# Kernel tuning notes

Measured on AMD Instinct MI355X. Metric: run time of the kernel, lower is better.

Reference implementation:

```python
import jax, jax.numpy as jnp
import numpy as np

EPS = 1e-8  # torch F.cosine_similarity eps


def _cosine_logits(emb, mem):
    # emb: [N, C], mem: [S, C] -> [N, S]
    num = emb @ mem.T
    denom = jnp.linalg.norm(emb, axis=1, keepdims=True) * jnp.linalg.norm(mem, axis=1)[None, :]
    return num / jnp.maximum(denom, EPS)


def setup_inputs() -> dict:
    key = jax.random.key(0)
    k1, k2, k3, k4 = jax.random.split(key, 4)
    N, S, C = 8192, 4096, 256
    return {
        "face": jax.random.normal(k1, (N, C), dtype=jnp.float32),
        "speech": jax.random.normal(k2, (N, C), dtype=jnp.float32),
        # init.normal_(mean=0, std=0.5)
        "speech_value_memory": 0.5 * jax.random.normal(k3, (S, C), dtype=jnp.float32),
        "face_key_memory": 0.5 * jax.random.normal(k4, (S, C), dtype=jnp.float32),
    }


def reference(face, speech, speech_value_memory, face_key_memory):
    # speech_encoder runs under torch.no_grad() -> stop_gradient; encoders abstracted as identity.
    speech_emb = jax.lax.stop_gradient(speech)
    face_emb = face

    speech_logits = _cosine_logits(speech_emb, speech_value_memory)      # [N, S]
    speech_address_log = jax.nn.log_softmax(speech_logits, axis=1)
    speech_address = jax.nn.softmax(speech_logits, axis=1)
    speech_emb_recall = speech_address @ speech_value_memory             # [N, C]

    face_logits = _cosine_logits(face_emb, face_key_memory)             # [N, S]
    face_address_log = jax.nn.log_softmax(face_logits, axis=1)
    face_address = jax.nn.softmax(face_logits, axis=1)
    face_emb_recall = face_address @ speech_value_memory                 # [N, C]

    return (speech_emb, speech_emb_recall, face_emb, face_emb_recall,
            speech_address_log, face_address_log)
```

## Files before the change

### kernel.cpp

```cpp
#include <hip/hip_runtime.h>
#include <hip/hip_bf16.h>
#include <cstdint>
#include <cstddef>

typedef __attribute__((ext_vector_type(8))) short bf16x8;
typedef __attribute__((ext_vector_type(4))) float f32x4;

static __device__ __forceinline__ unsigned short f2bf(float f) {
    union { float f; unsigned u; } v; v.f = f;
    return (unsigned short)((v.u + 0x7fffu + ((v.u >> 16) & 1u)) >> 16);
}
static __device__ __forceinline__ float bf2f(unsigned short h) {
    union { unsigned u; float f; } v; v.u = ((unsigned)h) << 16;
    return v.f;
}

static __device__ __forceinline__ void gld_lds16(const unsigned short* g, unsigned short* l) {
    __builtin_amdgcn_global_load_lds(
        (const __attribute__((address_space(1))) void*)g,
        (__attribute__((address_space(3))) void*)l, 16, 0, 0);
}

#define NC 2097152
#define SC 1048576
#define NS 33554432
#define SPLITS 4

__global__ __launch_bounds__(64) void rownorm_kernel(
    const float* __restrict__ face, const float* __restrict__ speech,
    const float* __restrict__ svm, const float* __restrict__ fkm,
    unsigned short* __restrict__ face_n, unsigned short* __restrict__ speech_n,
    unsigned short* __restrict__ svm_n, unsigned short* __restrict__ fkm_n,
    float* __restrict__ out_face, float* __restrict__ out_speech,
    unsigned short* __restrict__ svmT,
    float* __restrict__ out_srecall, float* __restrict__ out_frecall,
    float* __restrict__ sumexp)
{
    const int which = blockIdx.y;
    const int row   = blockIdx.x;
    const int lane  = threadIdx.x;

    if (which == 4) {
        const float4 z = make_float4(0.f, 0.f, 0.f, 0.f);
        *(float4*)(out_srecall + (size_t)row * 256 + lane * 4) = z;
        *(float4*)(out_frecall + (size_t)row * 256 + lane * 4) = z;
        if (lane < 2) sumexp[(size_t)lane * 8192 + row] = 0.f;
        return;
    }
    if (which >= 2 && row >= 4096) return;

    const float* in; unsigned short* nrm; float* cpy = nullptr; bool tr = false;
    if (which == 0)      { in = speech; nrm = speech_n; cpy = out_speech; }
    else if (which == 1) { in = face;   nrm = face_n;   cpy = out_face; }
    else if (which == 2) { in = svm;    nrm = svm_n;    tr = true; }
    else                 { in = fkm;    nrm = fkm_n; }

    const float4 v = *(const float4*)(in + (size_t)row * 256 + lane * 4);
    float ss = v.x * v.x + v.y * v.y + v.z * v.z + v.w * v.w;
    #pragma unroll
    for (int off = 32; off > 0; off >>= 1) ss += __shfl_xor(ss, off);
    const float rn = rsqrtf(ss);

    ushort4 o;
    o.x = f2bf(v.x * rn); o.y = f2bf(v.y * rn);
    o.z = f2bf(v.z * rn); o.w = f2bf(v.w * rn);
    *(ushort4*)(nrm + (size_t)row * 256 + lane * 4) = o;

    if (cpy) *(float4*)(cpy + (size_t)row * 256 + lane * 4) = v;

    if (tr) {
        const int c = lane * 4;
        svmT[(size_t)(c + 0) * 4096 + row] = f2bf(v.x);
        svmT[(size_t)(c + 1) * 4096 + row] = f2bf(v.y);
        svmT[(size_t)(c + 2) * 4096 + row] = f2bf(v.z);
        svmT[(size_t)(c + 3) * 4096 + row] = f2bf(v.w);
    }
}

__global__ __launch_bounds__(256) void gemm_logits_kernel(
    const unsigned short* __restrict__ speech_n,
    const unsigned short* __restrict__ face_n,
    const unsigned short* __restrict__ svm_n,
    const unsigned short* __restrict__ fkm_n,
    unsigned short* __restrict__ logits,
    float* __restrict__ sumexp)
{
    __shared__ unsigned short smem[128 * 32 * 2];
    unsigned short* As = smem;
    unsigned short* Bs = smem + 128 * 32;
    const int side = blockIdx.z;
    const unsigned short* A = side ? face_n : speech_n;
    const unsigned short* B = side ? fkm_n  : svm_n;
    unsigned short* Lg = logits + ((size_t)side * NS);

    const int row0 = blockIdx.y * 128;
    const int col0 = blockIdx.x * 128;
    const int tid  = threadIdx.x;
    const int wave = tid >> 6, lane = tid & 63;
    const int wm = (wave >> 1) * 64, wn = (wave & 1) * 64;
    const int quad = lane >> 4, r16 = lane & 15;

    const int r0 = tid >> 2,          cj0 = tid & 3;
    const int r1 = (tid + 256) >> 2,  cj1 = (tid + 256) & 3;

    f32x4 acc[4][4];
    #pragma unroll
    for (int i = 0; i < 4; i++)
        #pragma unroll
        for (int j = 0; j < 4; j++) acc[i][j] = 0.f;

    for (int k0 = 0; k0 < 256; k0 += 32) {
        gld_lds16(A + (size_t)(row0 + r0) * 256 + k0 + cj0 * 8, As + (size_t)(wave * 64) * 8);
        gld_lds16(B + (size_t)(col0 + r0) * 256 + k0 + cj0 * 8, Bs + (size_t)(wave * 64) * 8);
        gld_lds16(A + (size_t)(row0 + r1) * 256 + k0 + cj1 * 8, As + (size_t)(256 + wave * 64) * 8);
        gld_lds16(B + (size_t)(col0 + r1) * 256 + k0 + cj1 * 8, Bs + (size_t)(256 + wave * 64) * 8);
        __syncthreads();

        bf16x8 af[4], bfr[4];
        #pragma unroll
        for (int i = 0; i < 4; i++) {
            af[i]  = *(const bf16x8*)(&As[(wm + i * 16 + r16) * 32 + quad * 8]);
            bfr[i] = *(const bf16x8*)(&Bs[(wn + i * 16 + r16) * 32 + quad * 8]);
        }
        #pragma unroll
        for (int i = 0; i < 4; i++)
            #pragma unroll
            for (int j = 0; j < 4; j++)
                acc[i][j] = __builtin_amdgcn_mfma_f32_16x16x32_bf16(
                    af[i], bfr[j], acc[i][j], 0, 0, 0);
        __syncthreads();
    }

    #pragma unroll
    for (int i = 0; i < 4; i++) {
        #pragma unroll
        for (int rr = 0; rr < 4; rr++) {
            float s = 0.f;
            #pragma unroll
            for (int j = 0; j < 4; j++) s += __expf(acc[i][j][rr]);
            #pragma unroll
            for (int o = 8; o > 0; o >>= 1) s += __shfl_xor(s, o);
            if (r16 == 0)
                unsafeAtomicAdd(&sumexp[(size_t)side * 8192 + row0 + wm + i * 16 + quad * 4 + rr], s);
        }
    }

    unsigned short* tb = smem + wave * 2048;
    #pragma unroll
    for (int h = 0; h < 2; ++h) {
        #pragma unroll
        for (int i2 = 0; i2 < 2; ++i2)
            #pragma unroll
            for (int j = 0; j < 4; ++j)
                #pragma unroll
                for (int rr = 0; rr < 4; ++rr)
                    tb[(i2 * 16 + quad * 4 + rr) * 64 + j * 16 + r16] =
                        f2bf(acc[2 * h + i2][j][rr]);
        __syncthreads();
        #pragma unroll
        for (int p = 0; p < 4; ++p) {
            const int lrow = p * 8 + (lane >> 3);
            const int lcol = (lane & 7) * 8;
            const uint4 v = *(const uint4*)(tb + lrow * 64 + lcol);
            *(uint4*)(Lg + (size_t)(row0 + wm + h * 32 + lrow) * 4096 + col0 + wn + lcol) = v;
        }
        __syncthreads();
    }
}

__global__ __launch_bounds__(256) void gemm_recall_kernel(
    const unsigned short* __restrict__ logits,
    const float* __restrict__ sumexp,
    const unsigned short* __restrict__ BT,
    float* __restrict__ out_srecall, float* __restrict__ out_frecall,
    float* __restrict__ out_slog, float* __restrict__ out_flog)
{
    __shared__ unsigned short As[64 * 32];
    __shared__ unsigned short Bs[256 * 32];
    const int row0  = blockIdx.x * 64;
    const int split = blockIdx.y;
    const int side  = blockIdx.z;
    const unsigned short* A = logits + (size_t)side * NS;
    float* outp = side ? out_frecall : out_srecall;
    float* slog = side ? out_flog    : out_slog;
    const int kbase = split * (4096 / SPLITS);

    const int tid  = threadIdx.x;
    const int wave = tid >> 6, lane = tid & 63;
    const int wn = wave * 64;
    const int quad = lane >> 4, r16 = lane & 15;
    const int arow = tid >> 2, acj = tid & 3;
    const float myl = __logf(sumexp[(size_t)side * 8192 + row0 + arow]);
    float* slogp = slog + (size_t)(row0 + arow) * 4096 + acj * 8;

    f32x4 acc[4][4];
    #pragma unroll
    for (int i = 0; i < 4; i++)
        #pragma unroll
        for (int j = 0; j < 4; j++) acc[i][j] = 0.f;

    for (int k0 = kbase; k0 < kbase + 4096 / SPLITS; k0 += 32) {
        unsigned short vv[8];
        *(uint4*)vv = *(const uint4*)(A + (size_t)(row0 + arow) * 4096 + k0 + acj * 8);
        #pragma unroll
        for (int it = 0; it < 4; ++it) {
            const int c = tid + it * 256, r = c >> 2, cj = c & 3;
            gld_lds16(BT + (size_t)r * 4096 + k0 + cj * 8,
                      Bs + (size_t)(it * 256 + wave * 64) * 8);
        }
        float xs[8];
        #pragma unroll
        for (int k = 0; k < 8; k++) xs[k] = bf2f(vv[k]) - myl;
        f32x4 s0, s1;
        s0[0] = xs[0]; s0[1] = xs[1]; s0[2] = xs[2]; s0[3] = xs[3];
        s1[0] = xs[4]; s1[1] = xs[5]; s1[2] = xs[6]; s1[3] = xs[7];
        __builtin_nontemporal_store(s0, (f32x4*)(slogp + k0));
        __builtin_nontemporal_store(s1, (f32x4*)(slogp + k0 + 4));
        unsigned short pv[8];
        #pragma unroll
        for (int k = 0; k < 8; k++) pv[k] = f2bf(__expf(xs[k]));
        *(uint4*)(&As[arow * 32 + acj * 8]) = *(uint4*)pv;
        __syncthreads();

        bf16x8 af[4], bfr[4];
        #pragma unroll
        for (int i = 0; i < 4; i++) {
            af[i]  = *(const bf16x8*)(&As[(i * 16 + r16) * 32 + quad * 8]);
            bfr[i] = *(const bf16x8*)(&Bs[(wn + i * 16 + r16) * 32 + quad * 8]);
        }
        #pragma unroll
        for (int i = 0; i < 4; i++)
            #pragma unroll
            for (int j = 0; j < 4; j++)
                acc[i][j] = __builtin_amdgcn_mfma_f32_16x16x32_bf16(
                    af[i], bfr[j], acc[i][j], 0, 0, 0);
        __syncthreads();
    }

    #pragma unroll
    for (int i = 0; i < 4; i++) {
        #pragma unroll
        for (int j = 0; j < 4; j++) {
            const int r  = row0 + i * 16 + quad * 4;
            const int cc = wn + j * 16 + r16;
            #pragma unroll
            for (int rr = 0; rr < 4; rr++)
                unsafeAtomicAdd(&outp[(size_t)(r + rr) * 256 + cc], acc[i][j][rr]);
        }
    }
}

extern "C" void kernel_launch(void* const* d_in, const int* in_sizes, int n_in,
                              void* d_out, int out_size, void* d_ws, size_t ws_size,
                              hipStream_t stream) {
    const float* face   = (const float*)d_in[0];
    const float* speech = (const float*)d_in[1];
    const float* svm    = (const float*)d_in[2];
    const float* fkm    = (const float*)d_in[3];

    const int N = 8192, S = 4096, C = 256;
    float* out = (float*)d_out;
    float* out_speech  = out;
    float* out_srecall = out + (size_t)N * C;
    float* out_face    = out + 2 * (size_t)N * C;
    float* out_frecall = out + 3 * (size_t)N * C;
    float* out_slog    = out + 4 * (size_t)N * C;
    float* out_flog    = out_slog + (size_t)N * S;

    unsigned short* wsu = (unsigned short*)d_ws;
    unsigned short* speech_n = wsu;
    unsigned short* face_n   = speech_n + NC;
    unsigned short* svm_n    = face_n + NC;
    unsigned short* fkm_n    = svm_n + SC;
    unsigned short* svmT     = fkm_n + SC;
    unsigned short* logits   = svmT + SC;
    float* sumexp = (float*)(logits + 2 * (size_t)NS);

    dim3 g1(N, 5);
    rownorm_kernel<<<g1, 64, 0, stream>>>(face, speech, svm, fkm,
                                          face_n, speech_n, svm_n, fkm_n,
                                          out_face, out_speech, svmT,
                                          out_srecall, out_frecall, sumexp);

    dim3 g2(S / 128, N / 128, 2);
    gemm_logits_kernel<<<g2, 256, 0, stream>>>(speech_n, face_n, svm_n, fkm_n,
                                               logits, sumexp);

    dim3 g4(N / 64, SPLITS, 2);
    gemm_recall_kernel<<<g4, 256, 0, stream>>>(logits, sumexp, svmT,
                                               out_srecall, out_frecall,
                                               out_slog, out_flog);
}
```

Before: 471.2 us.

## Double GEMM K-tile to 64 with XOR-swizzled LDS and pack rownorm rows

Both the logits and recall GEMMs now stage 64-wide K tiles per barrier pair instead of 32, with an XOR swizzle on the 16-byte chunk index to avoid LDS bank conflicts. This halves the number of sync and load rounds, at the cost of more LDS per block, which may reduce occupancy. The recall kernel now has each thread handle two A rows per iteration. The logits epilogue drops its barriers because each wave uses a private staging region. The rownorm kernel packs four rows into each 256-thread block to cut launch and block overhead.

Result: slower. 495.2 us (+5.1%).

```diff
diff --git a/kernel.cpp b/kernel.cpp
--- a/kernel.cpp
+++ b/kernel.cpp
@@ -26,7 +26,7 @@
 #define NS 33554432
 #define SPLITS 4
 
-__global__ __launch_bounds__(64) void rownorm_kernel(
+__global__ __launch_bounds__(256) void rownorm_kernel(
     const float* __restrict__ face, const float* __restrict__ speech,
     const float* __restrict__ svm, const float* __restrict__ fkm,
     unsigned short* __restrict__ face_n, unsigned short* __restrict__ speech_n,
@@ -37,8 +37,9 @@
     float* __restrict__ sumexp)
 {
     const int which = blockIdx.y;
-    const int row   = blockIdx.x;
-    const int lane  = threadIdx.x;
+    const int sub   = threadIdx.x >> 6;
+    const int lane  = threadIdx.x & 63;
+    const int row   = blockIdx.x * 4 + sub;
 
     if (which == 4) {
         const float4 z = make_float4(0.f, 0.f, 0.f, 0.f);
@@ -85,9 +86,9 @@
     unsigned short* __restrict__ logits,
     float* __restrict__ sumexp)
 {
-    __shared__ unsigned short smem[128 * 32 * 2];
+    __shared__ unsigned short smem[2 * 128 * 64];
     unsigned short* As = smem;
-    unsigned short* Bs = smem + 128 * 32;
+    unsigned short* Bs = smem + 128 * 64;
     const int side = blockIdx.z;
     const unsigned short* A = side ? face_n : speech_n;
     const unsigned short* B = side ? fkm_n  : svm_n;
@@ -100,34 +101,42 @@
     const int wm = (wave >> 1) * 64, wn = (wave & 1) * 64;
     const int quad = lane >> 4, r16 = lane & 15;
 
-    const int r0 = tid >> 2,          cj0 = tid & 3;
-    const int r1 = (tid + 256) >> 2,  cj1 = (tid + 256) & 3;
-
     f32x4 acc[4][4];
     #pragma unroll
     for (int i = 0; i < 4; i++)
         #pragma unroll
         for (int j = 0; j < 4; j++) acc[i][j] = 0.f;
 
-    for (int k0 = 0; k0 < 256; k0 += 32) {
-        gld_lds16(A + (size_t)(row0 + r0) * 256 + k0 + cj0 * 8, As + (size_t)(wave * 64) * 8);
-        gld_lds16(B + (size_t)(col0 + r0) * 256 + k0 + cj0 * 8, Bs + (size_t)(wave * 64) * 8);
-        gld_lds16(A + (size_t)(row0 + r1) * 256 + k0 + cj1 * 8, As + (size_t)(256 + wave * 64) * 8);
-        gld_lds16(B + (size_t)(col0 + r1) * 256 + k0 + cj1 * 8, Bs + (size_t)(256 + wave * 64) * 8);
+    for (int k0 = 0; k0 < 256; k0 += 64) {
+        #pragma unroll
+        for (int it = 0; it < 4; ++it) {
+            const int c = tid + it * 256;
+            const int r = c >> 3, cj = c & 7;
+            const int sj = cj ^ (r & 7);
+            gld_lds16(A + (size_t)(row0 + r) * 256 + k0 + sj * 8,
+                      As + (size_t)(it * 256 + wave * 64) * 8);
+            gld_lds16(B + (size_t)(col0 + r) * 256 + k0 + sj * 8,
+                      Bs + (size_t)(it * 256 + wave * 64) * 8);
+        }
         __syncthreads();
 
-        bf16x8 af[4], bfr[4];
-        #pragma unroll
-        for (int i = 0; i < 4; i++) {
-            af[i]  = *(const bf16x8*)(&As[(wm + i * 16 + r16) * 32 + quad * 8]);
-            bfr[i] = *(const bf16x8*)(&Bs[(wn + i * 16 + r16) * 32 + quad * 8]);
-        }
-        #pragma unroll
-        for (int i = 0; i < 4; i++)
-            #pragma unroll
-            for (int j = 0; j < 4; j++)
-                acc[i][j] = __builtin_amdgcn_mfma_f32_16x16x32_bf16(
-                    af[i], bfr[j], acc[i][j], 0, 0, 0);
+        #pragma unroll
+        for (int kk = 0; kk < 2; ++kk) {
+            bf16x8 af[4], bfr[4];
+            #pragma unroll
+            for (int i = 0; i < 4; i++) {
+                const int ra = wm + i * 16 + r16;
+                af[i]  = *(const bf16x8*)(&As[ra * 64 + ((kk * 4 + quad) ^ (ra & 7)) * 8]);
+                const int rb = wn + i * 16 + r16;
+                bfr[i] = *(const bf16x8*)(&Bs[rb * 64 + ((kk * 4 + quad) ^ (rb & 7)) * 8]);
+            }
+            #pragma unroll
+            for (int i = 0; i < 4; i++)
+                #pragma unroll
+                for (int j = 0; j < 4; j++)
+                    acc[i][j] = __builtin_amdgcn_mfma_f32_16x16x32_bf16(
+                        af[i], bfr[j], acc[i][j], 0, 0, 0);
+        }
         __syncthreads();
     }
 
@@ -156,7 +165,6 @@
                 for (int rr = 0; rr < 4; ++rr)
                     tb[(i2 * 16 + quad * 4 + rr) * 64 + j * 16 + r16] =
                         f2bf(acc[2 * h + i2][j][rr]);
-        __syncthreads();
         #pragma unroll
         for (int p = 0; p < 4; ++p) {
             const int lrow = p * 8 + (lane >> 3);
@@ -164,7 +172,6 @@
             const uint4 v = *(const uint4*)(tb + lrow * 64 + lcol);
             *(uint4*)(Lg + (size_t)(row0 + wm + h * 32 + lrow) * 4096 + col0 + wn + lcol) = v;
         }
-        __syncthreads();
     }
 }
 
@@ -175,8 +182,8 @@
     float* __restrict__ out_srecall, float* __restrict__ out_frecall,
     float* __restrict__ out_slog, float* __restrict__ out_flog)
 {
-    __shared__ unsigned short As[64 * 32];
-    __shared__ unsigned short Bs[256 * 32];
+    __shared__ unsigned short As[64 * 64];
+    __shared__ unsigned short Bs[256 * 64];
     const int row0  = blockIdx.x * 64;
     const int split = blockIdx.y;
     const int side  = blockIdx.z;
@@ -189,9 +196,12 @@
     const int wave = tid >> 6, lane = tid & 63;
     const int wn = wave * 64;
     const int quad = lane >> 4, r16 = lane & 15;
-    const int arow = tid >> 2, acj = tid & 3;
-    const float myl = __logf(sumexp[(size_t)side * 8192 + row0 + arow]);
-    float* slogp = slog + (size_t)(row0 + arow) * 4096 + acj * 8;
+    const int ar  = tid >> 3, acj = tid & 7;
+    const float myl0 = __logf(sumexp[(size_t)side * 8192 + row0 + ar]);
+    const float myl1 = __logf(sumexp[(size_t)side * 8192 + row0 + ar + 32]);
+    float* slogp0 = slog + (size_t)(row0 + ar)      * 4096 + acj * 8;
+    float* slogp1 = slog + (size_t)(row0 + ar + 32) * 4096 + acj * 8;
+    const int asw = (acj ^ (ar & 7)) * 8;
 
     f32x4 acc[4][4];
     #pragma unroll
@@ -199,41 +209,60 @@
         #pragma unroll
         for (int j = 0; j < 4; j++) acc[i][j] = 0.f;
 
-    for (int k0 = kbase; k0 < kbase + 4096 / SPLITS; k0 += 32) {
-        unsigned short vv[8];
-        *(uint4*)vv = *(const uint4*)(A + (size_t)(row0 + arow) * 4096 + k0 + acj * 8);
-        #pragma unroll
-        for (int it = 0; it < 4; ++it) {
-            const int c = tid + it * 256, r = c >> 2, cj = c & 3;
-            gld_lds16(BT + (size_t)r * 4096 + k0 + cj * 8,
+    for (int k0 = kbase; k0 < kbase + 4096 / SPLITS; k0 += 64) {
+        uint4 a0 = *(const uint4*)(A + (size_t)(row0 + ar)      * 4096 + k0 + acj * 8);
+        uint4 a1 = *(const uint4*)(A + (size_t)(row0 + ar + 32) * 4096 + k0 + acj * 8);
+        #pragma unroll
+        for (int it = 0; it < 8; ++it) {
+            const int c = tid + it * 256, r = c >> 3, cj = c & 7;
+            gld_lds16(BT + (size_t)r * 4096 + k0 + (cj ^ (r & 7)) * 8,
                       Bs + (size_t)(it * 256 + wave * 64) * 8);
         }
-        float xs[8];
-        #pragma unroll
-        for (int k = 0; k < 8; k++) xs[k] = bf2f(vv[k]) - myl;
-        f32x4 s0, s1;
-        s0[0] = xs[0]; s0[1] = xs[1]; s0[2] = xs[2]; s0[3] = xs[3];
-        s1[0] = xs[4]; s1[1] = xs[5]; s1[2] = xs[6]; s1[3] = xs[7];
-        __builtin_nontemporal_store(s0, (f32x4*)(slogp + k0));
-        __builtin_nontemporal_store(s1, (f32x4*)(slogp + k0 + 4));
-        unsigned short pv[8];
-        #pragma unroll
-        for (int k = 0; k < 8; k++) pv[k] = f2bf(__expf(xs[k]));
-        *(uint4*)(&As[arow * 32 + acj * 8]) = *(uint4*)pv;
+        float xs0[8], xs1[8];
+        {
+            const unsigned short* v0 = (const unsigned short*)&a0;
+            const unsigned short* v1 = (const unsigned short*)&a1;
+            unsigned short p0[8], p1[8];
+            #pragma unroll
+            for (int k = 0; k < 8; k++) {
+                xs0[k] = bf2f(v0[k]) - myl0;
+                xs1[k] = bf2f(v1[k]) - myl1;
+                p0[k] = f2bf(__expf(xs0[k]));
+                p1[k] = f2bf(__expf(xs1[k]));
+            }
+            *(uint4*)(&As[ar * 64 + asw])        = *(uint4*)p0;
+            *(uint4*)(&As[(ar + 32) * 64 + asw]) = *(uint4*)p1;
+        }
         __syncthreads();
 
-        bf16x8 af[4], bfr[4];
-        #pragma unroll
-        for (int i = 0; i < 4; i++) {
-            af[i]  = *(const bf16x8*)(&As[(i * 16 + r16) * 32 + quad * 8]);
-            bfr[i] = *(const bf16x8*)(&Bs[(wn + i * 16 + r16) * 32 + quad * 8]);
-        }
-        #pragma unroll
-        for (int i = 0; i < 4; i++)
-            #pragma unroll
-            for (int j = 0; j < 4; j++)
-                acc[i][j] = __builtin_amdgcn_mfma_f32_16x16x32_bf16(
-                    af[i], bfr[j], acc[i][j], 0, 0, 0);
+        {
+            f32x4 s0, s1, s2, s3;
+            #pragma unroll
+            for (int k = 0; k < 4; k++) { s0[k] = xs0[k]; s1[k] = xs0[k + 4];
+                                          s2[k] = xs1[k]; s3[k] = xs1[k + 4]; }
+            __builtin_nontemporal_store(s0, (f32x4*)(slogp0 + k0));
+            __builtin_nontemporal_store(s1, (f32x4*)(slogp0 + k0 + 4));
+            __builtin_nontemporal_store(s2, (f32x4*)(slogp1 + k0));
+            __builtin_nontemporal_store(s3, (f32x4*)(slogp1 + k0 + 4));
+        }
+
+        #pragma unroll
+        for (int kk = 0; kk < 2; ++kk) {
+            bf16x8 af[4], bfr[4];
+            #pragma unroll
+            for (int i = 0; i < 4; i++) {
+                const int ra = i * 16 + r16;
+                af[i]  = *(const bf16x8*)(&As[ra * 64 + ((kk * 4 + quad) ^ (ra & 7)) * 8]);
+                const int rb = wn + i * 16 + r16;
+                bfr[i] = *(const bf16x8*)(&Bs[rb * 64 + ((kk * 4 + quad) ^ (rb & 7)) * 8]);
+            }
+            #pragma unroll
+            for (int i = 0; i < 4; i++)
+                #pragma unroll
+                for (int j = 0; j < 4; j++)
+                    acc[i][j] = __builtin_amdgcn_mfma_f32_16x16x32_bf16(
+                        af[i], bfr[j], acc[i][j], 0, 0, 0);
+        }
         __syncthreads();
     }
 
@@ -276,11 +305,11 @@
     unsigned short* logits   = svmT + SC;
     float* sumexp = (float*)(logits + 2 * (size_t)NS);
 
-    dim3 g1(N, 5);
-    rownorm_kernel<<<g1, 64, 0, stream>>>(face, speech, svm, fkm,
-                                          face_n, speech_n, svm_n, fkm_n,
-                                          out_face, out_speech, svmT,
-                                          out_srecall, out_frecall, sumexp);
+    dim3 g1(N / 4, 5);
+    rownorm_kernel<<<g1, 256, 0, stream>>>(face, speech, svm, fkm,
+                                           face_n, speech_n, svm_n, fkm_n,
+                                           out_face, out_speech, svmT,
+                                           out_srecall, out_frecall, sumexp);
 
     dim3 g2(S / 128, N / 128, 2);
     gemm_logits_kernel<<<g2, 256, 0, stream>>>(speech_n, face_n, svm_n, fkm_n,
```
